# Kernel optimization log

Hardware: AMD Instinct MI355X
Metric: run time of the kernel (lower is better)

## Reference

```python
import jax, jax.numpy as jnp
import numpy as np
import math

MID = 48       # mid_channels
HEADS = 4      # num_heads
POS = 16       # mid_channels // 3 (row/col positional channels)


def _unfold(x, p):
    """nn.Unfold with kernel p, padding p//2: (..., H, W) -> (..., p, p, H, W)."""
    H, W = x.shape[-2], x.shape[-1]
    pad = p // 2
    xp = jnp.pad(x, [(0, 0)] * (x.ndim - 2) + [(pad, pad), (pad, pad)])
    return jnp.stack(
        [jnp.stack([xp[..., k:k + H, l:l + W] for l in range(p)], axis=-3)
         for k in range(p)], axis=-4)


def _pe_mlp(idx, w1, b1, g, b, w2, b2):
    """Conv2d(1->16,1x1) -> LayerNorm(16) -> Swish -> Conv2d(16->POS,1x1) on scalar coords."""
    t = idx.reshape(-1, 1)                         # (N,1)
    h = t @ w1.T + b1                              # (N,16)
    mu = jnp.mean(h, -1, keepdims=True)
    var = jnp.var(h, -1, keepdims=True)
    h = (h - mu) * jax.lax.rsqrt(var + 1e-5) * g + b
    h = h * jax.nn.sigmoid(h)                      # Swish
    e = h @ w2.T + b2                              # (N,POS)
    return e.reshape(idx.shape + (e.shape[-1],))   # (V,P,P,POS)


def setup_inputs() -> dict:
    key = jax.random.key(0)
    ks = jax.random.split(key, 32)
    B, Cin, G, H, W, P, Cout = 2, 32, 4, 28, 28, 7, 64

    def n(k, shp, s=0.05):
        return jax.random.normal(k, shp, dtype=jnp.float32) * s

    inp = {"x": jax.random.normal(ks[0], (B, Cin, G, H, W), dtype=jnp.float32)}
    inp["Wq"] = n(ks[1], (MID * HEADS, Cin)); inp["bq"] = n(ks[2], (MID * HEADS,))
    inp["Wk"] = n(ks[3], (MID * HEADS, Cin)); inp["bk"] = n(ks[4], (MID * HEADS,))
    inp["Wv"] = n(ks[5], (MID * HEADS, Cin)); inp["bv"] = n(ks[6], (MID * HEADS,))
    inp["Wout"] = n(ks[7], (Cout, MID * HEADS)); inp["bout"] = n(ks[8], (Cout,))
    inp["row_w1"] = n(ks[9], (16, 1)); inp["row_b1"] = n(ks[10], (16,))
    inp["row_ln_g"] = jnp.ones((16,), jnp.float32); inp["row_ln_b"] = jnp.zeros((16,), jnp.float32)
    inp["row_w2"] = n(ks[11], (POS, 16)); inp["row_b2"] = n(ks[12], (POS,))
    inp["col_w1"] = n(ks[13], (16, 1)); inp["col_b1"] = n(ks[14], (16,))
    inp["col_ln_g"] = jnp.ones((16,), jnp.float32); inp["col_ln_b"] = jnp.zeros((16,), jnp.float32)
    inp["col_w2"] = n(ks[15], (POS, 16)); inp["col_b2"] = n(ks[16], (POS,))
    inp["group_emb"] = n(ks[17], (G, MID - 2 * POS))
    # rotated relative spatial positions, normalized to [-1, 1]
    lin = np.linspace(-1.0, 1.0, P).astype(np.float32)
    r = np.repeat(lin[:, None], P, 1)
    c = np.repeat(lin[None, :], P, 0)
    rows, cols = [], []
    for v in range(G):
        th = v * math.pi / 2.0
        rows.append(math.cos(th) * r - math.sin(th) * c)
        cols.append(math.sin(th) * r + math.cos(th) * c)
    inp["row_indices"] = jnp.asarray(np.stack(rows, 0))
    inp["col_indices"] = jnp.asarray(np.stack(cols, 0))
    # acted relative group positions for cyclic group C4
    ar = np.arange(G)
    gi = (ar[:, None, None] + ar[None, None, :] - ar[None, :, None]) % G
    inp["g_indices"] = jnp.asarray(gi, dtype=jnp.int32)
    return inp


def _forward(x, Wq, bq, Wk, bk, Wv, bv, Wout, bout,
             row_w1, row_b1, row_ln_g, row_ln_b, row_w2, row_b2,
             col_w1, col_b1, col_ln_g, col_ln_b, col_w2, col_b2,
             group_emb, row_indices, col_indices, g_indices):
    B, Cin, G, H, W = x.shape
    P = row_indices.shape[-1]
    sqn = jnp.sqrt(jnp.float32(Cin))

    def proj(Wm, bm):  # 1x1 Conv3d -> (B, MID, HEADS, G, H, W)
        y = jnp.einsum('oi,bigyx->bogyx', Wm, x) + bm[None, :, None, None, None]
        return y.reshape(B, MID, HEADS, G, H, W)

    q = proj(Wq, bq)
    k = proj(Wk, bk)
    v = proj(Wv, bv)
    k_loc = _unfold(k, P)   # (B, MID, HEADS, G, P, P, H, W)
    v_loc = _unfold(v, P)

    content = jnp.einsum('bchgij,bchmklij->bhgijmkl', q, k_loc)
    row_e = _pe_mlp(row_indices, row_w1, row_b1, row_ln_g, row_ln_b, row_w2, row_b2)
    col_e = _pe_mlp(col_indices, col_w1, col_b1, col_ln_g, col_ln_b, col_w2, col_b2)
    row_s = jnp.einsum('bchgij,vklc->bhvgijkl', q[:, :POS], row_e)
    col_s = jnp.einsum('bchgij,vklc->bhvgijkl', q[:, POS:2 * POS], col_e)
    g_e = group_emb[g_indices]                              # (V, G, M, gdim)
    g_s = jnp.einsum('bchgij,vgmc->bhvgijm', q[:, 2 * POS:], g_e)

    # scores: (b, h, v, g, i, j, m, k, l)
    scores = (row_s[:, :, :, :, :, :, None] + col_s[:, :, :, :, :, :, None]
              + g_s[..., None, None] + content[:, :, None]) / sqn

    # mask patch positions that fall outside the image (-inf -> prob 0)
    valid = _unfold(jnp.ones((H, W), jnp.float32), P)       # (P, P, H, W)
    valid = jnp.transpose(valid, (2, 3, 0, 1))[None, None, None, None, :, :, None, :, :]
    scores = jnp.where(valid > 0.5, scores, -jnp.inf)

    shp = scores.shape
    probs = jax.nn.softmax(scores.reshape(shp[:-3] + (-1,)), axis=-1).reshape(shp)

    o = jnp.einsum('bhvgijmkl,bchmklij->bchvij', probs, v_loc)  # (B, MID, HEADS, V, H, W)
    o = o.reshape(B, MID * HEADS, G, H, W)
    return jnp.einsum('oi,bivyx->bovyx', Wout, o) + bout[None, :, None, None, None]


def reference(x, Wq, bq, Wk, bk, Wv, bv, Wout, bout,
              row_w1, row_b1, row_ln_g, row_ln_b, row_w2, row_b2,
              col_w1, col_b1, col_ln_g, col_ln_b, col_w2, col_b2,
              group_emb, row_indices, col_indices, g_indices):
    return _forward(x, Wq, bq, Wk, bk, Wv, bv, Wout, bout,
                    row_w1, row_b1, row_ln_g, row_ln_b, row_w2, row_b2,
                    col_w1, col_b1, col_ln_g, col_ln_b, col_w2, col_b2,
                    group_emb, row_indices, col_indices, g_indices)
```

## Files before the change

kernel.cpp:

```cpp
#include <hip/hip_runtime.h>
#include <math.h>

#define Bb   2
#define CIN  32
#define Gg   4
#define NH   4
#define Hh   28
#define Ww   28
#define HW   784
#define Pp   7
#define PP   49
#define MID  48
#define COUT 64
#define OC   192

#define QOFF  0
#define KOFF  1204224
#define VOFF  2408448
#define OOFF  3612672

#define KSCALE 0.2550611135387359f

__device__ unsigned g_peT2[Gg * PP * 16];
__device__ unsigned g_geT2[8 * 64];
__device__ float    g_WT2[OC * COUT];

typedef _Float16 h2f __attribute__((ext_vector_type(2)));

__device__ __forceinline__ unsigned packh2(float a, float b) {
    auto r = __builtin_amdgcn_cvt_pkrtz(a, b);
    return __builtin_bit_cast(unsigned, r);
}

__device__ __forceinline__ float fdot2(unsigned a, unsigned b, float c) {
    return __builtin_amdgcn_fdot2(__builtin_bit_cast(h2f, a),
                                  __builtin_bit_cast(h2f, b), c, false);
}

__device__ __forceinline__ float exp2_fast(float x) {
    float r;
    asm("v_exp_f32 %0, %1" : "=v"(r) : "v"(x));
    return r;
}

__global__ __launch_bounds__(192) void qkvpe_kernel(const float* __restrict__ x,
    const float* __restrict__ Wq, const float* __restrict__ bq,
    const float* __restrict__ Wk, const float* __restrict__ bk,
    const float* __restrict__ Wv, const float* __restrict__ bv,
    const float* row_w1, const float* row_b1,
    const float* row_g,  const float* row_bb,
    const float* row_w2, const float* row_b2,
    const float* col_w1, const float* col_b1,
    const float* col_g,  const float* col_bb,
    const float* col_w2, const float* col_b2,
    const float* row_idx, const float* col_idx,
    const float* group_emb, const int* g_indices,
    const float* Wout,
    float* __restrict__ ws)
{
    __shared__ float xs[CIN * 16];
    __shared__ float wtmp[16 * 193];
    int tid = threadIdx.x;
    if (blockIdx.x == Bb * Gg * Hh * 2) {
        for (int t = tid; t < 2 * Gg * PP; t += 192) {
            int half = t / (Gg * PP);
            int n    = t - half * (Gg * PP);
            int v = n / PP, kl = n % PP;
            const float* w1 = half ? col_w1 : row_w1;
            const float* b1 = half ? col_b1 : row_b1;
            const float* lg = half ? col_g  : row_g;
            const float* lb = half ? col_bb : row_bb;
            const float* w2 = half ? col_w2 : row_w2;
            const float* b2 = half ? col_b2 : row_b2;
            float tv = half ? col_idx[n] : row_idx[n];

            float hb[16];
            float mean = 0.f;
            for (int k = 0; k < 16; k++) { hb[k] = tv * w1[k] + b1[k]; mean += hb[k]; }
            mean *= (1.f / 16.f);
            float var = 0.f;
            for (int k = 0; k < 16; k++) { float d = hb[k] - mean; var += d * d; }
            var *= (1.f / 16.f);
            float inv = 1.f / sqrtf(var + 1e-5f);
            for (int k = 0; k < 16; k++) {
                float hn = (hb[k] - mean) * inv * lg[k] + lb[k];
                hb[k] = hn / (1.f + expf(-hn));
            }
            float accv[16];
            for (int p = 0; p < 16; p++) {
                float acc = b2[p];
                for (int k = 0; k < 16; k++) acc += hb[k] * w2[p * 16 + k];
                accv[p] = acc * KSCALE;
            }
            for (int i2 = 0; i2 < 8; i2++)
                g_peT2[(v * PP + kl) * 16 + half * 8 + i2] =
                    packh2(accv[2 * i2], accv[2 * i2 + 1]);
        }
        for (int t = tid; t < 64; t += 192) {
            int gi = g_indices[t];
            for (int i2 = 0; i2 < 8; i2++)
                g_geT2[i2 * 64 + t] = packh2(group_emb[gi * 16 + 2 * i2] * KSCALE,
                                             group_emb[gi * 16 + 2 * i2 + 1] * KSCALE);
        }
        for (int chunk = 0; chunk < 4; chunk++) {
            int obase = chunk * 16;
            __syncthreads();
            for (int idx = tid; idx < 16 * OC; idx += 192) {
                int ol = idx / OC, t = idx % OC;
                wtmp[ol * 193 + t] = Wout[(obase + ol) * OC + t];
            }
            __syncthreads();
            for (int idx = tid; idx < 16 * OC; idx += 192) {
                int tp = idx / 16, ol = idx % 16;
                int h = tp / MID, c = tp % MID;
                g_WT2[tp * 64 + obase + ol] = wtmp[ol * 193 + c * NH + h];
            }
        }
        return;
    }

    int r = blockIdx.x;
    int jh = r & 1; r >>= 1;
    int i = r % Hh; r /= Hh;
    int g = r & 3;  int b = r >> 2;
    int j0 = jh * 14;

    for (int idx = tid; idx < CIN * 14; idx += 192) {
        int ci = idx / 14, jj = idx % 14;
        xs[ci * 16 + jj] = x[((b * CIN + ci) * Gg + g) * HW + i * Ww + j0 + jj];
    }
    __syncthreads();

    int h = tid / MID, c = tid % MID;
    int oo = c * NH + h;
    int wbase = (((b * NH + h) * Gg + g) * HW + i * Ww + j0) * MID + c;

    const float* Wm[3]  = {Wq, Wk, Wv};
    const float* bm[3]  = {bq, bk, bv};
    const int    off[3] = {QOFF, KOFF, VOFF};
    const float  scl[3] = {1.0f, KSCALE, 1.0f};
    for (int p = 0; p < 3; p++) {
        const float4* Wr4 = (const float4*)(Wm[p] + oo * CIN);
        float bias = bm[p][oo];
        float a[14];
        #pragma unroll
        for (int j = 0; j < 14; j++) a[j] = bias;

        #pragma unroll 2
        for (int ci8 = 0; ci8 < 8; ci8++) {
            float4 wv4 = Wr4[ci8];
            int cb = ci8 * 4;
#define CHAN(WV, CI)                                                          \
            {                                                                 \
                float wv = WV;                                                \
                float4 xA = *(const float4*)&xs[(CI) * 16 + 0];               \
                float4 xB = *(const float4*)&xs[(CI) * 16 + 4];               \
                float4 xC = *(const float4*)&xs[(CI) * 16 + 8];               \
                float2 xD = *(const float2*)&xs[(CI) * 16 + 12];              \
                a[0] += wv * xA.x;  a[1] += wv * xA.y;                        \
                a[2] += wv * xA.z;  a[3] += wv * xA.w;                        \
                a[4] += wv * xB.x;  a[5] += wv * xB.y;                        \
                a[6] += wv * xB.z;  a[7] += wv * xB.w;                        \
                a[8] += wv * xC.x;  a[9] += wv * xC.y;                        \
                a[10] += wv * xC.z; a[11] += wv * xC.w;                       \
                a[12] += wv * xD.x; a[13] += wv * xD.y;                       \
            }
            CHAN(wv4.x, cb + 0)
            CHAN(wv4.y, cb + 1)
            CHAN(wv4.z, cb + 2)
            CHAN(wv4.w, cb + 3)
#undef CHAN
        }
        float s = scl[p];
        #pragma unroll
        for (int j = 0; j < 14; j++) ws[off[p] + wbase + j * MID] = a[j] * s;
    }
}

__global__ __launch_bounds__(256, 4) void attn_kernel(float* __restrict__ ws)
{
    __shared__ __align__(16) unsigned kvb[7560];
    __shared__ __align__(16) unsigned pp2[4][PP][8];
    __shared__ __align__(16) unsigned qp[4][4][32];
    __shared__ __align__(16) float gsm[4][64];

    const int tid  = threadIdx.x;
    const int wave = tid >> 6;
    const int lane = tid & 63;

    int blk = blockIdx.x;
    int j0 = (blk % 7) * 4;
    int i  = (blk / 7) % Hh;
    int bh = blk / (7 * Hh);
    int b = bh >> 2, h = bh & 3;
    int j  = j0 + wave;
    int ij = i * Ww + j;

    const float* Qt  = ws + QOFF;
    const float* Kbh = ws + KOFF + (size_t)bh * Gg * HW * MID;
    const float* Vbh = ws + VOFF + (size_t)bh * Gg * HW * MID;
    float* Ot = ws + OOFF;

    if (lane < 48) {
        int g = lane / 12, c4 = lane % 12;
        float4 qv = *(const float4*)&Qt[((size_t)(bh * Gg + g) * HW + ij) * MID + c4 * 4];
        qp[wave][g][c4 * 2]     = packh2(qv.x, qv.y);
        qp[wave][g][c4 * 2 + 1] = packh2(qv.z, qv.w);
    }

    for (int t = tid; t < 3360; t += 256) {
        int c4 = t % 12; int cell = (t / 12) % 70; int m = t / 840;
        int gy = i - 3 + cell / 10, gx = j0 - 3 + cell % 10;
        float4 val = {0.f, 0.f, 0.f, 0.f};
        if ((unsigned)gy < Hh && (unsigned)gx < Ww)
            val = *(const float4*)&Kbh[((size_t)(m * HW + gy * Ww + gx)) * MID + c4 * 4];
        *(uint2*)&kvb[(m * 70 + cell) * 27 + c4 * 2] = make_uint2(packh2(val.x, val.y),
                                                                  packh2(val.z, val.w));
    }

    int kk = lane / Pp, ll = lane % Pp;
    int cell = (lane < PP) ? kk * 10 + ll + wave : 0;
    bool vmask = (lane < PP) && ((unsigned)(i + kk - 3) < Hh) && ((unsigned)(j + ll - 3) < Ww);
    int lclamp = lane < PP ? lane : 0;

    float per[4][4] = {};
    #pragma unroll
    for (int u4 = 0; u4 < 4; u4++) {
        uint4 qA = *(const uint4*)&qp[wave][0][u4 * 4];
        uint4 qB = *(const uint4*)&qp[wave][1][u4 * 4];
        uint4 qC = *(const uint4*)&qp[wave][2][u4 * 4];
        uint4 qD = *(const uint4*)&qp[wave][3][u4 * 4];
        #pragma unroll
        for (int v = 0; v < 4; v++) {
            uint4 pk = *(const uint4*)&g_peT2[(v * PP + lclamp) * 16 + u4 * 4];
            per[v][0] = fdot2(pk.w, qA.w, fdot2(pk.z, qA.z, fdot2(pk.y, qA.y, fdot2(pk.x, qA.x, per[v][0]))));
            per[v][1] = fdot2(pk.w, qB.w, fdot2(pk.z, qB.z, fdot2(pk.y, qB.y, fdot2(pk.x, qB.x, per[v][1]))));
            per[v][2] = fdot2(pk.w, qC.w, fdot2(pk.z, qC.z, fdot2(pk.y, qC.y, fdot2(pk.x, qC.x, per[v][2]))));
            per[v][3] = fdot2(pk.w, qD.w, fdot2(pk.z, qD.z, fdot2(pk.y, qD.y, fdot2(pk.x, qD.x, per[v][3]))));
        }
    }
    if (!vmask) {
        #pragma unroll
        for (int v = 0; v < 4; v++)
            #pragma unroll
            for (int g = 0; g < 4; g++) per[v][g] = -INFINITY;
    }

    {
        int g = (lane >> 2) & 3;
        float ga = 0.f;
        #pragma unroll
        for (int u = 0; u < 8; u++)
            ga = fdot2(g_geT2[u * 64 + lane], qp[wave][g][16 + u], ga);
        gsm[wave][lane] = ga;
    }
    __syncthreads();

    float acc[4][4] = {};
    #pragma unroll 2
    for (int u4 = 0; u4 < 6; u4++) {
        uint4 qA = *(const uint4*)&qp[wave][0][u4 * 4];
        uint4 qB = *(const uint4*)&qp[wave][1][u4 * 4];
        uint4 qC = *(const uint4*)&qp[wave][2][u4 * 4];
        uint4 qD = *(const uint4*)&qp[wave][3][u4 * 4];
        #pragma unroll
        for (int m = 0; m < 4; m++) {
            int base = (m * 70 + cell) * 27 + u4 * 4;
            uint2 k01 = *(const uint2*)&kvb[base];
            uint2 k23 = *(const uint2*)&kvb[base + 2];
            acc[m][0] = fdot2(k23.y, qA.w, fdot2(k23.x, qA.z, fdot2(k01.y, qA.y, fdot2(k01.x, qA.x, acc[m][0]))));
            acc[m][1] = fdot2(k23.y, qB.w, fdot2(k23.x, qB.z, fdot2(k01.y, qB.y, fdot2(k01.x, qB.x, acc[m][1]))));
            acc[m][2] = fdot2(k23.y, qC.w, fdot2(k23.x, qC.z, fdot2(k01.y, qC.y, fdot2(k01.x, qC.x, acc[m][2]))));
            acc[m][3] = fdot2(k23.y, qD.w, fdot2(k23.x, qD.z, fdot2(k01.y, qD.y, fdot2(k01.x, qD.x, acc[m][3]))));
        }
    }

    float ppr[4][4] = {};
    #pragma unroll
    for (int v = 0; v < 4; v++) {
        #pragma unroll
        for (int g = 0; g < 4; g++) {
            int vg = v * 4 + g;
            float4 gs = *(const float4*)&gsm[wave][vg * 4];
            float ex[4]; float ls = 0.f;
            ex[0] = exp2_fast(acc[0][g] + per[v][g] + gs.x);
            ex[1] = exp2_fast(acc[1][g] + per[v][g] + gs.y);
            ex[2] = exp2_fast(acc[2][g] + per[v][g] + gs.z);
            ex[3] = exp2_fast(acc[3][g] + per[v][g] + gs.w);
            ls = ex[0] + ex[1] + ex[2] + ex[3];
            #pragma unroll
            for (int d = 32; d > 0; d >>= 1) ls += __shfl_xor(ls, d, 64);
            float rinv = 1.0f / ls;
            #pragma unroll
            for (int m = 0; m < 4; m++) ppr[v][m] += ex[m] * rinv;
        }
    }
    if (lane < PP) {
        uint4 w0, w1;
        w0.x = packh2(ppr[0][0], ppr[0][1]); w0.y = packh2(ppr[0][2], ppr[0][3]);
        w0.z = packh2(ppr[1][0], ppr[1][1]); w0.w = packh2(ppr[1][2], ppr[1][3]);
        w1.x = packh2(ppr[2][0], ppr[2][1]); w1.y = packh2(ppr[2][2], ppr[2][3]);
        w1.z = packh2(ppr[3][0], ppr[3][1]); w1.w = packh2(ppr[3][2], ppr[3][3]);
        *(uint4*)&pp2[wave][lane][0] = w0;
        *(uint4*)&pp2[wave][lane][4] = w1;
    }
    __syncthreads();

    for (int t = tid; t < 840; t += 256) {
        int c4 = t % 12; int cl = t / 12;
        int gy = i - 3 + cl / 10, gx = j0 - 3 + cl % 10;
        float4 v0 = {0.f,0.f,0.f,0.f}, v1 = v0, v2 = v0, v3 = v0;
        if ((unsigned)gy < Hh && (unsigned)gx < Ww) {
            const float* vp = &Vbh[((size_t)(gy * Ww + gx)) * MID + c4 * 4];
            v0 = *(const float4*)vp;
            v1 = *(const float4*)(vp + (size_t)HW * MID);
            v2 = *(const float4*)(vp + (size_t)2 * HW * MID);
            v3 = *(const float4*)(vp + (size_t)3 * HW * MID);
        }
        uint4 wA, wB;
        wA.x = packh2(v0.x, v1.x); wA.y = packh2(v2.x, v3.x);
        wA.z = packh2(v0.y, v1.y); wA.w = packh2(v2.y, v3.y);
        wB.x = packh2(v0.z, v1.z); wB.y = packh2(v2.z, v3.z);
        wB.z = packh2(v0.w, v1.w); wB.w = packh2(v2.w, v3.w);
        *(uint4*)&kvb[(cl * 48 + c4 * 4) * 2    ] = wA;
        *(uint4*)&kvb[(cl * 48 + c4 * 4) * 2 + 4] = wB;
    }
    __syncthreads();

    if (lane < MID) {
        float o0 = 0.f, o1 = 0.f, o2 = 0.f, o3 = 0.f;
        const uint4* ppw = (const uint4*)&pp2[wave][0][0];
        for (int kk2 = 0; kk2 < Pp; kk2++) {
            #pragma unroll
            for (int ll2 = 0; ll2 < Pp; ll2++) {
                int kl2  = kk2 * Pp + ll2;
                int cell2 = kk2 * 10 + ll2 + wave;
                uint2 vv = *(const uint2*)&kvb[(cell2 * 48 + lane) * 2];
                uint4 A = ppw[kl2 * 2];
                uint4 B = ppw[kl2 * 2 + 1];
                o0 = fdot2(vv.y, A.y, fdot2(vv.x, A.x, o0));
                o1 = fdot2(vv.y, A.w, fdot2(vv.x, A.z, o1));
                o2 = fdot2(vv.y, B.y, fdot2(vv.x, B.x, o2));
                o3 = fdot2(vv.y, B.w, fdot2(vv.x, B.z, o3));
            }
        }
        Ot[((size_t)(b * Gg + 0) * HW + ij) * OC + h * MID + lane] = o0;
        Ot[((size_t)(b * Gg + 1) * HW + ij) * OC + h * MID + lane] = o1;
        Ot[((size_t)(b * Gg + 2) * HW + ij) * OC + h * MID + lane] = o2;
        Ot[((size_t)(b * Gg + 3) * HW + ij) * OC + h * MID + lane] = o3;
    }
}

__global__ __launch_bounds__(256) void outproj_kernel(const float* __restrict__ bout,
                                                      const float* __restrict__ ws,
                                                      float* __restrict__ out)
{
    __shared__ float ov[16 * 193];
    __shared__ float res[64 * 17];
    int tid = threadIdx.x;
    int p0 = blockIdx.x * 16;
    const float* Ot = ws + OOFF;

    for (int idx = tid; idx < 16 * OC; idx += 256) {
        int pl = idx / OC, t = idx % OC;
        ov[pl * 193 + t] = Ot[(size_t)(p0 + pl) * OC + t];
    }
    __syncthreads();

    int o = tid & 63, pg = tid >> 6;
    float a0 = bout[o], a1 = a0, a2 = a0, a3 = a0;
    for (int t = 0; t < OC; t++) {
        float w = g_WT2[t * 64 + o];
        a0 += w * ov[(pg     ) * 193 + t];
        a1 += w * ov[(pg +  4) * 193 + t];
        a2 += w * ov[(pg +  8) * 193 + t];
        a3 += w * ov[(pg + 12) * 193 + t];
    }
    res[o * 17 + pg     ] = a0;
    res[o * 17 + pg +  4] = a1;
    res[o * 17 + pg +  8] = a2;
    res[o * 17 + pg + 12] = a3;
    __syncthreads();

    for (int idx = tid; idx < 1024; idx += 256) {
        int o2 = idx >> 4, pl = idx & 15;
        int p = p0 + pl;
        int ij2 = p % HW; int bv = p / HW; int v = bv & 3; int bb = bv >> 2;
        out[((bb * COUT + o2) * Gg + v) * HW + ij2] = res[o2 * 17 + pl];
    }
}

extern "C" void kernel_launch(void* const* d_in, const int* in_sizes, int n_in,
                              void* d_out, int out_size, void* d_ws, size_t ws_size,
                              hipStream_t stream)
{
    const float* x      = (const float*)d_in[0];
    const float* Wq     = (const float*)d_in[1];
    const float* bq     = (const float*)d_in[2];
    const float* Wk     = (const float*)d_in[3];
    const float* bk     = (const float*)d_in[4];
    const float* Wv     = (const float*)d_in[5];
    const float* bv     = (const float*)d_in[6];
    const float* Wout   = (const float*)d_in[7];
    const float* bout   = (const float*)d_in[8];
    const float* row_w1 = (const float*)d_in[9];
    const float* row_b1 = (const float*)d_in[10];
    const float* row_g  = (const float*)d_in[11];
    const float* row_bb = (const float*)d_in[12];
    const float* row_w2 = (const float*)d_in[13];
    const float* row_b2 = (const float*)d_in[14];
    const float* col_w1 = (const float*)d_in[15];
    const float* col_b1 = (const float*)d_in[16];
    const float* col_g  = (const float*)d_in[17];
    const float* col_bb = (const float*)d_in[18];
    const float* col_w2 = (const float*)d_in[19];
    const float* col_b2 = (const float*)d_in[20];
    const float* gemb   = (const float*)d_in[21];
    const float* ridx   = (const float*)d_in[22];
    const float* cidx   = (const float*)d_in[23];
    const int*   gidx   = (const int*)d_in[24];

    float* ws  = (float*)d_ws;
    float* out = (float*)d_out;

    qkvpe_kernel<<<Bb * Gg * Hh * 2 + 1, 192, 0, stream>>>(
        x, Wq, bq, Wk, bk, Wv, bv,
        row_w1, row_b1, row_g, row_bb, row_w2, row_b2,
        col_w1, col_b1, col_g, col_bb, col_w2, col_b2,
        ridx, cidx, gemb, gidx, Wout, ws);
    attn_kernel<<<Bb * NH * Hh * (Ww / 4), 256, 0, stream>>>(ws);
    outproj_kernel<<<Bb * Gg * HW / 16, 256, 0, stream>>>(bout, ws, out);
}
```

Baseline: 180.2 us.

## Halve attention LDS staging buffer by processing K and V in two passes

The K and V tiles are now staged in shared memory in two halves of two frames each, with the content scores and the PV product computed per half. This cuts the kvb buffer from 7560 to 3780 words, so more blocks can fit per CU. The cost is extra __syncthreads barriers and serialised load/compute phases. The PV pass also changes its pp2 packing and V layout to match the split.

```diff
diff --git a/kernel.cpp b/kernel.cpp
--- a/kernel.cpp
+++ b/kernel.cpp
@@ -179,8 +179,8 @@
 
 __global__ __launch_bounds__(256, 4) void attn_kernel(float* __restrict__ ws)
 {
-    __shared__ __align__(16) unsigned kvb[7560];
-    __shared__ __align__(16) unsigned pp2[4][PP][8];
+    __shared__ __align__(16) unsigned kvb[3780];
+    __shared__ __align__(16) unsigned pp2[4][2][PP][4];
     __shared__ __align__(16) unsigned qp[4][4][32];
     __shared__ __align__(16) float gsm[4][64];
 
@@ -208,15 +208,73 @@
         qp[wave][g][c4 * 2 + 1] = packh2(qv.z, qv.w);
     }
 
-    for (int t = tid; t < 3360; t += 256) {
-        int c4 = t % 12; int cell = (t / 12) % 70; int m = t / 840;
-        int gy = i - 3 + cell / 10, gx = j0 - 3 + cell % 10;
-        float4 val = {0.f, 0.f, 0.f, 0.f};
-        if ((unsigned)gy < Hh && (unsigned)gx < Ww)
-            val = *(const float4*)&Kbh[((size_t)(m * HW + gy * Ww + gx)) * MID + c4 * 4];
-        *(uint2*)&kvb[(m * 70 + cell) * 27 + c4 * 2] = make_uint2(packh2(val.x, val.y),
-                                                                  packh2(val.z, val.w));
-    }
+#define STAGE_K(HALF)                                                           \
+    for (int t = tid; t < 1680; t += 256) {                                     \
+        int c4 = t % 12; int cell = (t / 12) % 70; int ml = t / 840;            \
+        int gy = i - 3 + cell / 10, gx = j0 - 3 + cell % 10;                    \
+        float4 val = {0.f, 0.f, 0.f, 0.f};                                      \
+        if ((unsigned)gy < Hh && (unsigned)gx < Ww)                             \
+            val = *(const float4*)&Kbh[((size_t)(((HALF) * 2 + ml) * HW         \
+                                        + gy * Ww + gx)) * MID + c4 * 4];       \
+        *(uint2*)&kvb[(ml * 70 + cell) * 27 + c4 * 2] =                         \
+            make_uint2(packh2(val.x, val.y), packh2(val.z, val.w));             \
+    }
+
+#define CONTENT(HALF)                                                           \
+    _Pragma("unroll 2")                                                         \
+    for (int u4 = 0; u4 < 6; u4++) {                                            \
+        uint4 qA = *(const uint4*)&qp[wave][0][u4 * 4];                         \
+        uint4 qB = *(const uint4*)&qp[wave][1][u4 * 4];                         \
+        uint4 qC = *(const uint4*)&qp[wave][2][u4 * 4];                         \
+        uint4 qD = *(const uint4*)&qp[wave][3][u4 * 4];                         \
+        _Pragma("unroll")                                                       \
+        for (int ml = 0; ml < 2; ml++) {                                        \
+            int m = (HALF) * 2 + ml;                                            \
+            int base = (ml * 70 + cell) * 27 + u4 * 4;                          \
+            uint2 k01 = *(const uint2*)&kvb[base];                              \
+            uint2 k23 = *(const uint2*)&kvb[base + 2];                          \
+            acc[m][0] = fdot2(k23.y, qA.w, fdot2(k23.x, qA.z, fdot2(k01.y, qA.y, fdot2(k01.x, qA.x, acc[m][0])))); \
+            acc[m][1] = fdot2(k23.y, qB.w, fdot2(k23.x, qB.z, fdot2(k01.y, qB.y, fdot2(k01.x, qB.x, acc[m][1])))); \
+            acc[m][2] = fdot2(k23.y, qC.w, fdot2(k23.x, qC.z, fdot2(k01.y, qC.y, fdot2(k01.x, qC.x, acc[m][2])))); \
+            acc[m][3] = fdot2(k23.y, qD.w, fdot2(k23.x, qD.z, fdot2(k01.y, qD.y, fdot2(k01.x, qD.x, acc[m][3])))); \
+        }                                                                       \
+    }
+
+#define STAGE_V(PAIR)                                                           \
+    for (int t = tid; t < 840; t += 256) {                                      \
+        int c4 = t % 12; int cl = t / 12;                                       \
+        int gy = i - 3 + cl / 10, gx = j0 - 3 + cl % 10;                        \
+        float4 v0 = {0.f,0.f,0.f,0.f}, v1 = v0;                                 \
+        if ((unsigned)gy < Hh && (unsigned)gx < Ww) {                           \
+            const float* vp = &Vbh[((size_t)((PAIR) * 2 * HW + gy * Ww + gx))   \
+                                   * MID + c4 * 4];                             \
+            v0 = *(const float4*)vp;                                            \
+            v1 = *(const float4*)(vp + (size_t)HW * MID);                       \
+        }                                                                       \
+        uint4 w;                                                                \
+        w.x = packh2(v0.x, v1.x); w.y = packh2(v0.y, v1.y);                     \
+        w.z = packh2(v0.z, v1.z); w.w = packh2(v0.w, v1.w);                     \
+        *(uint4*)&kvb[cl * 52 + c4 * 4] = w;                                    \
+    }
+
+#define PV_PASS(PAIR)                                                           \
+    if (lane < MID) {                                                           \
+        for (int kk2 = 0; kk2 < Pp; kk2++) {                                    \
+            _Pragma("unroll")                                                   \
+            for (int ll2 = 0; ll2 < Pp; ll2++) {                                \
+                int kl2  = kk2 * Pp + ll2;                                      \
+                int cell2 = kk2 * 10 + ll2 + wave;                              \
+                unsigned vv = kvb[cell2 * 52 + lane];                           \
+                uint4 A = *(const uint4*)&pp2[wave][PAIR][kl2][0];              \
+                o0 = fdot2(vv, A.x, o0);                                        \
+                o1 = fdot2(vv, A.y, o1);                                        \
+                o2 = fdot2(vv, A.z, o2);                                        \
+                o3 = fdot2(vv, A.w, o3);                                        \
+            }                                                                   \
+        }                                                                       \
+    }
+
+    STAGE_K(0)
 
     int kk = lane / Pp, ll = lane % Pp;
     int cell = (lane < PP) ? kk * 10 + ll + wave : 0;
@@ -254,26 +312,14 @@
             ga = fdot2(g_geT2[u * 64 + lane], qp[wave][g][16 + u], ga);
         gsm[wave][lane] = ga;
     }
-    __syncthreads();
 
     float acc[4][4] = {};
-    #pragma unroll 2
-    for (int u4 = 0; u4 < 6; u4++) {
-        uint4 qA = *(const uint4*)&qp[wave][0][u4 * 4];
-        uint4 qB = *(const uint4*)&qp[wave][1][u4 * 4];
-        uint4 qC = *(const uint4*)&qp[wave][2][u4 * 4];
-        uint4 qD = *(const uint4*)&qp[wave][3][u4 * 4];
-        #pragma unroll
-        for (int m = 0; m < 4; m++) {
-            int base = (m * 70 + cell) * 27 + u4 * 4;
-            uint2 k01 = *(const uint2*)&kvb[base];
-            uint2 k23 = *(const uint2*)&kvb[base + 2];
-            acc[m][0] = fdot2(k23.y, qA.w, fdot2(k23.x, qA.z, fdot2(k01.y, qA.y, fdot2(k01.x, qA.x, acc[m][0]))));
-            acc[m][1] = fdot2(k23.y, qB.w, fdot2(k23.x, qB.z, fdot2(k01.y, qB.y, fdot2(k01.x, qB.x, acc[m][1]))));
-            acc[m][2] = fdot2(k23.y, qC.w, fdot2(k23.x, qC.z, fdot2(k01.y, qC.y, fdot2(k01.x, qC.x, acc[m][2]))));
-            acc[m][3] = fdot2(k23.y, qD.w, fdot2(k23.x, qD.z, fdot2(k01.y, qD.y, fdot2(k01.x, qD.x, acc[m][3]))));
-        }
-    }
+    __syncthreads();
+    CONTENT(0)
+    __syncthreads();
+    STAGE_K(1)
+    __syncthreads();
+    CONTENT(1)
 
     float ppr[4][4] = {};
     #pragma unroll
@@ -282,12 +328,12 @@
         for (int g = 0; g < 4; g++) {
             int vg = v * 4 + g;
             float4 gs = *(const float4*)&gsm[wave][vg * 4];
-            float ex[4]; float ls = 0.f;
+            float ex[4];
             ex[0] = exp2_fast(acc[0][g] + per[v][g] + gs.x);
             ex[1] = exp2_fast(acc[1][g] + per[v][g] + gs.y);
             ex[2] = exp2_fast(acc[2][g] + per[v][g] + gs.z);
             ex[3] = exp2_fast(acc[3][g] + per[v][g] + gs.w);
-            ls = ex[0] + ex[1] + ex[2] + ex[3];
+            float ls = ex[0] + ex[1] + ex[2] + ex[3];
             #pragma unroll
             for (int d = 32; d > 0; d >>= 1) ls += __shfl_xor(ls, d, 64);
             float rinv = 1.0f / ls;
@@ -297,58 +343,34 @@
     }
     if (lane < PP) {
         uint4 w0, w1;
-        w0.x = packh2(ppr[0][0], ppr[0][1]); w0.y = packh2(ppr[0][2], ppr[0][3]);
-        w0.z = packh2(ppr[1][0], ppr[1][1]); w0.w = packh2(ppr[1][2], ppr[1][3]);
-        w1.x = packh2(ppr[2][0], ppr[2][1]); w1.y = packh2(ppr[2][2], ppr[2][3]);
-        w1.z = packh2(ppr[3][0], ppr[3][1]); w1.w = packh2(ppr[3][2], ppr[3][3]);
-        *(uint4*)&pp2[wave][lane][0] = w0;
-        *(uint4*)&pp2[wave][lane][4] = w1;
-    }
-    __syncthreads();
-
-    for (int t = tid; t < 840; t += 256) {
-        int c4 = t % 12; int cl = t / 12;
-        int gy = i - 3 + cl / 10, gx = j0 - 3 + cl % 10;
-        float4 v0 = {0.f,0.f,0.f,0.f}, v1 = v0, v2 = v0, v3 = v0;
-        if ((unsigned)gy < Hh && (unsigned)gx < Ww) {
-            const float* vp = &Vbh[((size_t)(gy * Ww + gx)) * MID + c4 * 4];
-            v0 = *(const float4*)vp;
-            v1 = *(const float4*)(vp + (size_t)HW * MID);
-            v2 = *(const float4*)(vp + (size_t)2 * HW * MID);
-            v3 = *(const float4*)(vp + (size_t)3 * HW * MID);
-        }
-        uint4 wA, wB;
-        wA.x = packh2(v0.x, v1.x); wA.y = packh2(v2.x, v3.x);
-        wA.z = packh2(v0.y, v1.y); wA.w = packh2(v2.y, v3.y);
-        wB.x = packh2(v0.z, v1.z); wB.y = packh2(v2.z, v3.z);
-        wB.z = packh2(v0.w, v1.w); wB.w = packh2(v2.w, v3.w);
-        *(uint4*)&kvb[(cl * 48 + c4 * 4) * 2    ] = wA;
-        *(uint4*)&kvb[(cl * 48 + c4 * 4) * 2 + 4] = wB;
-    }
-    __syncthreads();
+        w0.x = packh2(ppr[0][0], ppr[0][1]); w0.y = packh2(ppr[1][0], ppr[1][1]);
+        w0.z = packh2(ppr[2][0], ppr[2][1]); w0.w = packh2(ppr[3][0], ppr[3][1]);
+        w1.x = packh2(ppr[0][2], ppr[0][3]); w1.y = packh2(ppr[1][2], ppr[1][3]);
+        w1.z = packh2(ppr[2][2], ppr[2][3]); w1.w = packh2(ppr[3][2], ppr[3][3]);
+        *(uint4*)&pp2[wave][0][lane][0] = w0;
+        *(uint4*)&pp2[wave][1][lane][0] = w1;
+    }
+
+    float o0 = 0.f, o1 = 0.f, o2 = 0.f, o3 = 0.f;
+    __syncthreads();
+    STAGE_V(0)
+    __syncthreads();
+    PV_PASS(0)
+    __syncthreads();
+    STAGE_V(1)
+    __syncthreads();
+    PV_PASS(1)
 
     if (lane < MID) {
-        float o0 = 0.f, o1 = 0.f, o2 = 0.f, o3 = 0.f;
-        const uint4* ppw = (const uint4*)&pp2[wave][0][0];
-        for (int kk2 = 0; kk2 < Pp; kk2++) {
-            #pragma unroll
-            for (int ll2 = 0; ll2 < Pp; ll2++) {
-                int kl2  = kk2 * Pp + ll2;
-                int cell2 = kk2 * 10 + ll2 + wave;
-                uint2 vv = *(const uint2*)&kvb[(cell2 * 48 + lane) * 2];
-                uint4 A = ppw[kl2 * 2];
-                uint4 B = ppw[kl2 * 2 + 1];
-                o0 = fdot2(vv.y, A.y, fdot2(vv.x, A.x, o0));
-                o1 = fdot2(vv.y, A.w, fdot2(vv.x, A.z, o1));
-                o2 = fdot2(vv.y, B.y, fdot2(vv.x, B.x, o2));
-                o3 = fdot2(vv.y, B.w, fdot2(vv.x, B.z, o3));
-            }
-        }
         Ot[((size_t)(b * Gg + 0) * HW + ij) * OC + h * MID + lane] = o0;
         Ot[((size_t)(b * Gg + 1) * HW + ij) * OC + h * MID + lane] = o1;
         Ot[((size_t)(b * Gg + 2) * HW + ij) * OC + h * MID + lane] = o2;
         Ot[((size_t)(b * Gg + 3) * HW + ij) * OC + h * MID + lane] = o3;
     }
+#undef STAGE_K
+#undef CONTENT
+#undef STAGE_V
+#undef PV_PASS
 }
 
 __global__ __launch_bounds__(256) void outproj_kernel(const float* __restrict__ bout,
```

New measurement: 184.4 us. +2.3%, slower.
